# Kernel tuning notes

Hardware: AMD Instinct MI355X
Metric: run time of the kernel (lower is better)

## Reference

```python
import jax, jax.numpy as jnp
import numpy as np


def setup_inputs() -> dict:
    key = jax.random.key(0)
    k1, k2 = jax.random.split(key)
    state_variable = jax.random.normal(k1, (32, 512, 512, 1), dtype=jnp.float32)
    velocity_field = jax.random.normal(k2, (32, 512, 512, 2), dtype=jnp.float32)
    return {"state_variable": state_variable, "velocity_field": velocity_field}


def reference(state_variable, velocity_field):
    # Even-size filter [-1, 1]: pad (0, 1) on H and W, SYMMETRIC (reflect-with-edge).
    p = jnp.pad(state_variable, ((0, 0), (0, 1), (0, 1), (0, 0)), mode="symmetric")
    # Diagonal 2x2 conv filters reduce to forward differences per channel.
    # dy[b,i,j,c] = p[b,i+1,j,c] - p[b,i,j,c]; dx[b,i,j,c] = p[b,i,j+1,c] - p[b,i,j,c]
    dy = p[:, 1:, :-1, :] - p[:, :-1, :-1, :]   # [B, H, W, C]
    dx = p[:, :-1, 1:, :] - p[:, :-1, :-1, :]   # [B, H, W, C]
    spatial_deriv = jnp.concatenate([dy, dx], axis=-1)  # [B, H, W, 2C]
    advect = jnp.sum(spatial_deriv * velocity_field, axis=-1, keepdims=True)  # [B, H, W, 1]
    return advect
```

## Files before the change

### kernel.cpp

```cpp
#include <hip/hip_runtime.h>


#define H 512
#define W 512
#define PLANE (H * W)

typedef float f4 __attribute__((ext_vector_type(4)));

__global__ __launch_bounds__(1024) void advect_kernel(
    const float* __restrict__ s,
    const float* __restrict__ v,
    float* __restrict__ out)
{
    const int t = blockIdx.x * blockDim.x + threadIdx.x;
    const int q = t << 2;
    const int b   = q >> 18;
    const int rem = q & (PLANE - 1);
    const int i   = rem >> 9;
    const int j   = rem & (W - 1);

    const float* srow   = s + (size_t)b * PLANE + (size_t)i * W;
    const int    idn    = (i + 1 < H) ? (i + 1) : (H - 1);
    const float* srowdn = s + (size_t)b * PLANE + (size_t)idn * W;

    const f4 s0 = *reinterpret_cast<const f4*>(srow + j);
    const f4 sd = *reinterpret_cast<const f4*>(srowdn + j);
    const float s4 = (j + 4 < W) ? srow[j + 4] : s0.w;

    const f4 v01 = *reinterpret_cast<const f4*>(v + (size_t)q * 2);
    const f4 v23 = *reinterpret_cast<const f4*>(v + (size_t)q * 2 + 4);

    f4 o;
    o.x = (sd.x - s0.x) * v01.x + (s0.y - s0.x) * v01.y;
    o.y = (sd.y - s0.y) * v01.z + (s0.z - s0.y) * v01.w;
    o.z = (sd.z - s0.z) * v23.x + (s0.w - s0.z) * v23.y;
    o.w = (sd.w - s0.w) * v23.z + (s4   - s0.w) * v23.w;

    *reinterpret_cast<f4*>(out + q) = o;
}

extern "C" void kernel_launch(void* const* d_in, const int* in_sizes, int n_in,
                              void* d_out, int out_size, void* d_ws, size_t ws_size,
                              hipStream_t stream) {
    const float* s = (const float*)d_in[0];
    const float* v = (const float*)d_in[1];
    float* out = (float*)d_out;

    const int n_pixels = 32 * PLANE;
    const int threads = n_pixels / 4;
    const int block = 1024;
    const int grid = threads / block;
    advect_kernel<<<grid, block, 0, stream>>>(s, v, out);
}
```

Measured before the change: 25.05 us.

## Use persistent grid-stride loop with register prefetch and 2-pixel per-lane loads

Measured after the change: 25.30 us. About the same (+1.0%).

```diff
diff --git a/kernel.cpp b/kernel.cpp
--- a/kernel.cpp
+++ b/kernel.cpp
@@ -4,39 +4,71 @@
 #define H 512
 #define W 512
 #define PLANE (H * W)
+#define TOTAL_PX (32 * PLANE)
+#define NWG 512
+#define BLK 1024
+#define ITERS 4
+#define STRIDE (NWG * BLK * 4)
 
+typedef float f2 __attribute__((ext_vector_type(2)));
 typedef float f4 __attribute__((ext_vector_type(4)));
 
-__global__ __launch_bounds__(1024) void advect_kernel(
+struct PxLoads { f2 s0, sd; float s2; f4 v; };
+
+__device__ __forceinline__ PxLoads load_pair(const float* __restrict__ s,
+                                             const float* __restrict__ v, int p) {
+    const int b   = p >> 18;
+    const int rem = p & (PLANE - 1);
+    const int i   = rem >> 9;
+    const int j   = rem & (W - 1);
+    const float* srow = s + (size_t)b * PLANE + (size_t)i * W;
+    const float* srd  = srow + ((i + 1 < H) ? W : 0);
+    PxLoads L;
+    L.s0 = *reinterpret_cast<const f2*>(srow + j);
+    L.sd = *reinterpret_cast<const f2*>(srd + j);
+    L.s2 = srow[(j + 2 < W) ? j + 2 : W - 1];
+    L.v  = *reinterpret_cast<const f4*>(v + (size_t)p * 2);
+    return L;
+}
+
+__device__ __forceinline__ f2 compute(const PxLoads& L) {
+    f2 o;
+    o.x = (L.sd.x - L.s0.x) * L.v.x + (L.s0.y - L.s0.x) * L.v.y;
+    o.y = (L.sd.y - L.s0.y) * L.v.z + (L.s2   - L.s0.y) * L.v.w;
+    return o;
+}
+
+__global__ __launch_bounds__(BLK, 8) void advect_kernel(
     const float* __restrict__ s,
     const float* __restrict__ v,
     float* __restrict__ out)
 {
-    const int t = blockIdx.x * blockDim.x + threadIdx.x;
-    const int q = t << 2;
-    const int b   = q >> 18;
-    const int rem = q & (PLANE - 1);
-    const int i   = rem >> 9;
-    const int j   = rem & (W - 1);
+    const int tid  = blockIdx.x * BLK + threadIdx.x;
+    const int wav  = tid >> 6;
+    const int lane = tid & 63;
 
-    const float* srow   = s + (size_t)b * PLANE + (size_t)i * W;
-    const int    idn    = (i + 1 < H) ? (i + 1) : (H - 1);
-    const float* srowdn = s + (size_t)b * PLANE + (size_t)idn * W;
+    int pA = (wav << 8) + (lane << 1);
+    int pB = pA + 128;
 
-    const f4 s0 = *reinterpret_cast<const f4*>(srow + j);
-    const f4 sd = *reinterpret_cast<const f4*>(srowdn + j);
-    const float s4 = (j + 4 < W) ? srow[j + 4] : s0.w;
+    PxLoads A = load_pair(s, v, pA);
+    PxLoads B = load_pair(s, v, pB);
 
-    const f4 v01 = *reinterpret_cast<const f4*>(v + (size_t)q * 2);
-    const f4 v23 = *reinterpret_cast<const f4*>(v + (size_t)q * 2 + 4);
-
-    f4 o;
-    o.x = (sd.x - s0.x) * v01.x + (s0.y - s0.x) * v01.y;
-    o.y = (sd.y - s0.y) * v01.z + (s0.z - s0.y) * v01.w;
-    o.z = (sd.z - s0.z) * v23.x + (s0.w - s0.z) * v23.y;
-    o.w = (sd.w - s0.w) * v23.z + (s4   - s0.w) * v23.w;
-
-    *reinterpret_cast<f4*>(out + q) = o;
+    #pragma unroll
+    for (int k = 0; k < ITERS; ++k) {
+        PxLoads A2, B2;
+        if (k + 1 < ITERS) {
+            A2 = load_pair(s, v, pA + STRIDE);
+            B2 = load_pair(s, v, pB + STRIDE);
+        }
+        const f2 oA = compute(A);
+        const f2 oB = compute(B);
+        *reinterpret_cast<f2*>(out + pA) = oA;
+        *reinterpret_cast<f2*>(out + pB) = oB;
+        pA += STRIDE;
+        pB += STRIDE;
+        A = A2;
+        B = B2;
+    }
 }
 
 extern "C" void kernel_launch(void* const* d_in, const int* in_sizes, int n_in,
@@ -46,9 +78,5 @@
     const float* v = (const float*)d_in[1];
     float* out = (float*)d_out;
 
-    const int n_pixels = 32 * PLANE;
-    const int threads = n_pixels / 4;
-    const int block = 1024;
-    const int grid = threads / block;
-    advect_kernel<<<grid, block, 0, stream>>>(s, v, out);
+    advect_kernel<<<NWG, BLK, 0, stream>>>(s, v, out);
 }
```
